# Optimization experiments

Measured on AMD Instinct MI355X. Metric: run time of the kernel, lower is better.

## Reference

```python
import jax, jax.numpy as jnp
import numpy as np

TEMPERATURE = 0.5


def setup_inputs() -> dict:
    key = jax.random.key(0)
    k1, k2 = jax.random.split(key)
    N, D = 4096, 256
    z_i = jax.random.normal(k1, (N, D), dtype=jnp.float32)
    z_j = jax.random.normal(k2, (N, D), dtype=jnp.float32)
    return {"z_i": z_i, "z_j": z_j}


def reference(z_i, z_j):
    N = z_i.shape[0]
    z = jnp.concatenate([z_i, z_j], axis=0)            # (2N, D)
    sim = (z @ z.T) / TEMPERATURE                       # (2N, 2N)
    # mask self-similarity on the diagonal
    diag = jnp.eye(2 * N, dtype=bool)
    sim = jnp.where(diag, -jnp.inf, sim)
    # positive pair labels: i <-> i+N
    labels = jnp.concatenate([jnp.arange(N, 2 * N), jnp.arange(0, N)])
    logp = jax.nn.log_softmax(sim, axis=-1)             # (2N, 2N)
    loss = -jnp.mean(jnp.take_along_axis(logp, labels[:, None], axis=-1))
    return loss
```

## Files before the change

kernel.cpp:

```cpp
#include <hip/hip_runtime.h>
#include <hip/hip_bf16.h>


typedef __bf16 bf16x8 __attribute__((ext_vector_type(8)));
typedef __bf16 bf16x4 __attribute__((ext_vector_type(4)));
typedef float  f32x16 __attribute__((ext_vector_type(16)));

#define NPAIR 4096
#define NROW  8192
#define DIM   256
#define STRIPS 8
#define RBLK  16384
#define SQSCALE 1.6986437f
#define LN2F    0.6931471805599453f
#define M2      176.0f

__global__ __launch_bounds__(256) void k_convert(const float* __restrict__ zi,
                                                 const float* __restrict__ zj,
                                                 __bf16* __restrict__ Zf,
                                                 float* __restrict__ pos,
                                                 float* __restrict__ out) {
    const int w = threadIdx.x >> 6, lane = threadIdx.x & 63;
    const int r = blockIdx.x * 4 + w;
    if (blockIdx.x == 0 && threadIdx.x == 0) out[0] = 0.0f;
    const float4 vi = *(const float4*)(zi + r * DIM + lane * 4);
    const float4 vj = *(const float4*)(zj + r * DIM + lane * 4);
    bf16x4 bi, bj;
    bi[0] = (__bf16)(vi.x * SQSCALE); bi[1] = (__bf16)(vi.y * SQSCALE);
    bi[2] = (__bf16)(vi.z * SQSCALE); bi[3] = (__bf16)(vi.w * SQSCALE);
    bj[0] = (__bf16)(vj.x * SQSCALE); bj[1] = (__bf16)(vj.y * SQSCALE);
    bj[2] = (__bf16)(vj.z * SQSCALE); bj[3] = (__bf16)(vj.w * SQSCALE);
    const int t = lane >> 2, h = (lane >> 1) & 1, inner = (lane & 1) * 8;
    char* Zb = (char*)Zf;
    *(bf16x4*)(Zb + (size_t)(r >> 5) * RBLK + t * 1024 + h * 512 + (r & 31) * 16 + inner) = bi;
    const int r2 = r + NPAIR;
    *(bf16x4*)(Zb + (size_t)(r2 >> 5) * RBLK + t * 1024 + h * 512 + (r2 & 31) * 16 + inner) = bj;
    float d = vi.x * vj.x + vi.y * vj.y + vi.z * vj.z + vi.w * vj.w;
    #pragma unroll
    for (int m = 32; m >= 1; m >>= 1) d += __shfl_xor(d, m);
    if (lane == 0) pos[r] = 2.0f * d;
}

__global__ __launch_bounds__(512) void k_lse(const __bf16* __restrict__ Zf,
                                             float* __restrict__ Lpart) {
    const int strip = blockIdx.x >> 6;
    const int rb    = blockIdx.x & 63;
    const int tid   = threadIdx.x;
    const int wave  = tid >> 6;
    const int wr    = wave & 3;
    const int wc    = wave >> 2;
    const int lane  = tid & 63, lm = lane & 31, half = lane >> 5;
    const int laneoff = half * 512 + lm * 16;

    __shared__ char smem[65536];
    {
        const char* src = (const char*)Zf + (size_t)rb * 4 * RBLK + tid * 16;
        char* dst = smem + tid * 16;
        #pragma unroll
        for (int it = 0; it < 8; it++)
            *(int4*)(dst + it * 8192) = *(const int4*)(src + it * 8192);
    }
    __syncthreads();

    const char* Bl    = smem + wr * RBLK + laneoff;
    const char* Abase = (const char*)Zf + (size_t)(strip * 32 + wc * 2) * RBLK + laneoff;
    const int rowblk  = rb * 4 + wr;

    float l = 0.0f;

    for (int ph = 0; ph < 8; ph++) {
        const char* Ap = Abase + (size_t)ph * 4 * RBLK;
        f32x16 acc0 = (f32x16)(0.0f);
        f32x16 acc1 = (f32x16)(0.0f);

        bf16x8 a0 = *(const bf16x8*)(Ap);
        bf16x8 a1 = *(const bf16x8*)(Ap + RBLK);
        bf16x8 b  = *(const bf16x8*)(Bl);
        #pragma unroll
        for (int t = 0; t < 16; t++) {
            bf16x8 na0, na1, nb;
            if (t < 15) {
                na0 = *(const bf16x8*)(Ap + (t + 1) * 1024);
                na1 = *(const bf16x8*)(Ap + RBLK + (t + 1) * 1024);
                nb  = *(const bf16x8*)(Bl + (t + 1) * 1024);
            }
            acc0 = __builtin_amdgcn_mfma_f32_32x32x16_bf16(a0, b, acc0, 0, 0, 0);
            acc1 = __builtin_amdgcn_mfma_f32_32x32x16_bf16(a1, b, acc1, 0, 0, 0);
            a0 = na0; a1 = na1; b = nb;
        }

        const int cb0 = strip * 32 + ph * 4 + wc * 2;
        float ssum = 0.0f;
        if (cb0 == rowblk) {
            #pragma unroll
            for (int rg = 0; rg < 16; rg++) {
                const int c_local = (rg & 3) + 8 * (rg >> 2) + 4 * half;
                ssum += (c_local == lm) ? 0.0f : __builtin_exp2f(acc0[rg] - M2);
            }
        } else {
            #pragma unroll
            for (int rg = 0; rg < 16; rg++) ssum += __builtin_exp2f(acc0[rg] - M2);
        }
        if (cb0 + 1 == rowblk) {
            #pragma unroll
            for (int rg = 0; rg < 16; rg++) {
                const int c_local = (rg & 3) + 8 * (rg >> 2) + 4 * half;
                ssum += (c_local == lm) ? 0.0f : __builtin_exp2f(acc1[rg] - M2);
            }
        } else {
            #pragma unroll
            for (int rg = 0; rg < 16; rg++) ssum += __builtin_exp2f(acc1[rg] - M2);
        }
        l += ssum;
    }

    l += __shfl_xor(l, 32);

    __syncthreads();
    float* part = (float*)smem;
    if (half == 0) part[wc * 128 + wr * 32 + lm] = l;
    __syncthreads();
    if (tid < 128)
        Lpart[strip * NROW + rb * 128 + tid] = part[tid] + part[128 + tid];
}

__global__ __launch_bounds__(256) void k_final(const float* __restrict__ Lpart,
                                               const float* __restrict__ pos,
                                               float* __restrict__ out) {
    __shared__ float red[256];
    const int t = threadIdx.x;
    const int r = blockIdx.x * 256 + t;
    float l = 0.0f;
    #pragma unroll
    for (int s = 0; s < STRIPS; s++) l += Lpart[s * NROW + r];
    const float lse = (M2 + __builtin_log2f(l)) * LN2F;
    red[t] = lse - pos[r & (NPAIR - 1)];
    __syncthreads();
    for (int ofs = 128; ofs > 0; ofs >>= 1) {
        if (t < ofs) red[t] += red[t + ofs];
        __syncthreads();
    }
    if (t == 0) atomicAdd(out, red[0] / (float)NROW);
}

extern "C" void kernel_launch(void* const* d_in, const int* in_sizes, int n_in,
                              void* d_out, int out_size, void* d_ws, size_t ws_size,
                              hipStream_t stream) {
    const float* zi = (const float*)d_in[0];
    const float* zj = (const float*)d_in[1];
    __bf16* Zf   = (__bf16*)d_ws;
    float* pos   = (float*)((char*)d_ws + (size_t)NROW * DIM * 2);
    float* Lpart = pos + NPAIR;

    k_convert<<<NPAIR / 4, 256, 0, stream>>>(zi, zj, Zf, pos, (float*)d_out);
    k_lse<<<64 * STRIPS, 512, 0, stream>>>(Zf, Lpart);
    k_final<<<NROW / 256, 256, 0, stream>>>(Lpart, pos, (float*)d_out);
}
```

Baseline: 106.2 us.

## Keep row operand in registers and double-buffer column tiles via LDS DMA

Restructures the LSE kernel so each wave holds its two row blocks in registers, while column blocks are streamed into a double-buffered LDS tile with global_load_lds and barriers. The previous version cached rows in LDS and read columns directly from global memory. Strips double to 16 and blocks shrink to 256 threads with two blocks per CU, so work is spread more finely. The cost is higher register pressure from 32 bf16x8 operand registers per lane and a barrier per phase.

After: 104.3 us. Within noise of the previous version (-1.8%).

```diff
diff --git a/kernel.cpp b/kernel.cpp
--- a/kernel.cpp
+++ b/kernel.cpp
@@ -9,7 +9,7 @@
 #define NPAIR 4096
 #define NROW  8192
 #define DIM   256
-#define STRIPS 8
+#define STRIPS 16
 #define RBLK  16384
 #define SQSCALE 1.6986437f
 #define LN2F    0.6931471805599453f
@@ -41,87 +41,108 @@
     if (lane == 0) pos[r] = 2.0f * d;
 }
 
-__global__ __launch_bounds__(512) void k_lse(const __bf16* __restrict__ Zf,
-                                             float* __restrict__ Lpart) {
-    const int strip = blockIdx.x >> 6;
-    const int rb    = blockIdx.x & 63;
+__global__ __launch_bounds__(256, 2) void k_lse(const __bf16* __restrict__ Zf,
+                                                float* __restrict__ Lpart) {
+    const int bx    = blockIdx.x;
+    const int rb    = bx & 31;
+    const int strip = bx >> 5;
     const int tid   = threadIdx.x;
-    const int wave  = tid >> 6;
-    const int wr    = wave & 3;
-    const int wc    = wave >> 2;
+    const int w     = tid >> 6;
     const int lane  = tid & 63, lm = lane & 31, half = lane >> 5;
     const int laneoff = half * 512 + lm * 16;
+    const int R0 = rb * 8 + w * 2, R1 = R0 + 1;
 
-    __shared__ char smem[65536];
+    __shared__ __align__(16) char smem[32768];
+    const char* Zb = (const char*)Zf;
+
+    bf16x8 B0[16], B1[16];
     {
-        const char* src = (const char*)Zf + (size_t)rb * 4 * RBLK + tid * 16;
-        char* dst = smem + tid * 16;
+        const char* g0 = Zb + (size_t)R0 * RBLK + laneoff;
+        const char* g1 = Zb + (size_t)R1 * RBLK + laneoff;
         #pragma unroll
-        for (int it = 0; it < 8; it++)
-            *(int4*)(dst + it * 8192) = *(const int4*)(src + it * 8192);
+        for (int t = 0; t < 16; t++) {
+            B0[t] = *(const bf16x8*)(g0 + t * 1024);
+            B1[t] = *(const bf16x8*)(g1 + t * 1024);
+        }
     }
-    __syncthreads();
 
-    const char* Bl    = smem + wr * RBLK + laneoff;
-    const char* Abase = (const char*)Zf + (size_t)(strip * 32 + wc * 2) * RBLK + laneoff;
-    const int rowblk  = rb * 4 + wr;
+    const char* Acol = Zb + (size_t)strip * 16 * RBLK;
 
-    float l = 0.0f;
+    #define STAGE(bufsel, phidx) do {                                              \
+        const char* _s = Acol + (size_t)(phidx) * RBLK + tid * 16;                 \
+        char*       _d = smem + (bufsel) * 16384 + tid * 16;                       \
+        _Pragma("unroll")                                                          \
+        for (int _q = 0; _q < 4; _q++)                                             \
+            __builtin_amdgcn_global_load_lds(                                      \
+                (const __attribute__((address_space(1))) unsigned int*)(_s + _q * 4096), \
+                (__attribute__((address_space(3))) unsigned int*)(_d + _q * 4096), \
+                16, 0, 0);                                                         \
+    } while (0)
 
-    for (int ph = 0; ph < 8; ph++) {
-        const char* Ap = Abase + (size_t)ph * 4 * RBLK;
+    STAGE(0, 0);
+    float l0 = 0.0f, l1 = 0.0f;
+
+    #pragma unroll 2
+    for (int ph = 0; ph < 16; ph++) {
+        if (ph < 15) {
+            STAGE((ph + 1) & 1, ph + 1);
+            asm volatile("s_waitcnt vmcnt(4)" ::: "memory");
+        } else {
+            asm volatile("s_waitcnt vmcnt(0)" ::: "memory");
+        }
+        __builtin_amdgcn_s_barrier();
+        __builtin_amdgcn_sched_barrier(0);
+
+        const char* Ab = smem + (ph & 1) * 16384 + laneoff;
         f32x16 acc0 = (f32x16)(0.0f);
         f32x16 acc1 = (f32x16)(0.0f);
-
-        bf16x8 a0 = *(const bf16x8*)(Ap);
-        bf16x8 a1 = *(const bf16x8*)(Ap + RBLK);
-        bf16x8 b  = *(const bf16x8*)(Bl);
+        __builtin_amdgcn_s_setprio(1);
+        bf16x8 a = *(const bf16x8*)(Ab);
         #pragma unroll
         for (int t = 0; t < 16; t++) {
-            bf16x8 na0, na1, nb;
-            if (t < 15) {
-                na0 = *(const bf16x8*)(Ap + (t + 1) * 1024);
-                na1 = *(const bf16x8*)(Ap + RBLK + (t + 1) * 1024);
-                nb  = *(const bf16x8*)(Bl + (t + 1) * 1024);
-            }
-            acc0 = __builtin_amdgcn_mfma_f32_32x32x16_bf16(a0, b, acc0, 0, 0, 0);
-            acc1 = __builtin_amdgcn_mfma_f32_32x32x16_bf16(a1, b, acc1, 0, 0, 0);
-            a0 = na0; a1 = na1; b = nb;
+            bf16x8 na;
+            if (t < 15) na = *(const bf16x8*)(Ab + (t + 1) * 1024);
+            acc0 = __builtin_amdgcn_mfma_f32_32x32x16_bf16(a, B0[t], acc0, 0, 0, 0);
+            acc1 = __builtin_amdgcn_mfma_f32_32x32x16_bf16(a, B1[t], acc1, 0, 0, 0);
+            a = na;
         }
+        __builtin_amdgcn_s_setprio(0);
 
-        const int cb0 = strip * 32 + ph * 4 + wc * 2;
-        float ssum = 0.0f;
-        if (cb0 == rowblk) {
+        const int cb = strip * 16 + ph;
+        float s0 = 0.0f, s1 = 0.0f;
+        if (cb == R0) {
             #pragma unroll
             for (int rg = 0; rg < 16; rg++) {
-                const int c_local = (rg & 3) + 8 * (rg >> 2) + 4 * half;
-                ssum += (c_local == lm) ? 0.0f : __builtin_exp2f(acc0[rg] - M2);
+                const int cl = (rg & 3) + 8 * (rg >> 2) + 4 * half;
+                s0 += (cl == lm) ? 0.0f : __builtin_exp2f(acc0[rg] - M2);
             }
         } else {
             #pragma unroll
-            for (int rg = 0; rg < 16; rg++) ssum += __builtin_exp2f(acc0[rg] - M2);
+            for (int rg = 0; rg < 16; rg++) s0 += __builtin_exp2f(acc0[rg] - M2);
         }
-        if (cb0 + 1 == rowblk) {
+        if (cb == R1) {
             #pragma unroll
             for (int rg = 0; rg < 16; rg++) {
-                const int c_local = (rg & 3) + 8 * (rg >> 2) + 4 * half;
-                ssum += (c_local == lm) ? 0.0f : __builtin_exp2f(acc1[rg] - M2);
+                const int cl = (rg & 3) + 8 * (rg >> 2) + 4 * half;
+                s1 += (cl == lm) ? 0.0f : __builtin_exp2f(acc1[rg] - M2);
             }
         } else {
             #pragma unroll
-            for (int rg = 0; rg < 16; rg++) ssum += __builtin_exp2f(acc1[rg] - M2);
+            for (int rg = 0; rg < 16; rg++) s1 += __builtin_exp2f(acc1[rg] - M2);
         }
-        l += ssum;
+        l0 += s0; l1 += s1;
+
+        __builtin_amdgcn_sched_barrier(0);
+        __builtin_amdgcn_s_barrier();
     }
+    #undef STAGE
 
-    l += __shfl_xor(l, 32);
-
-    __syncthreads();
-    float* part = (float*)smem;
-    if (half == 0) part[wc * 128 + wr * 32 + lm] = l;
-    __syncthreads();
-    if (tid < 128)
-        Lpart[strip * NROW + rb * 128 + tid] = part[tid] + part[128 + tid];
+    l0 += __shfl_xor(l0, 32);
+    l1 += __shfl_xor(l1, 32);
+    if (half == 0) {
+        Lpart[strip * NROW + R0 * 32 + lm] = l0;
+        Lpart[strip * NROW + R1 * 32 + lm] = l1;
+    }
 }
 
 __global__ __launch_bounds__(256) void k_final(const float* __restrict__ Lpart,
@@ -153,6 +174,6 @@
     float* Lpart = pos + NPAIR;
 
     k_convert<<<NPAIR / 4, 256, 0, stream>>>(zi, zj, Zf, pos, (float*)d_out);
-    k_lse<<<64 * STRIPS, 512, 0, stream>>>(Zf, Lpart);
+    k_lse<<<32 * STRIPS, 256, 0, stream>>>(Zf, Lpart);
     k_final<<<NROW / 256, 256, 0, stream>>>(Lpart, pos, (float*)d_out);
 }
```
